# Performance work log

Hardware: AMD Instinct MI355X
Metric: run time of the kernel (lower is better)

The kernel has to match this reference:

```python
import jax, jax.numpy as jnp
import numpy as np

# Static multi-scale pyramid (H, W per level); Nv = sum(H*W) = 13294
SPATIAL = np.array([[100, 100], [50, 50], [25, 25], [13, 13]], dtype=np.int64)
B, C, NH, NL, NP = 2, 256, 8, 4, 4
D = C // NH
TOT = NH * NL * NP


def setup_inputs() -> dict:
    key = jax.random.key(0)
    ks = jax.random.split(key, 10)
    Nv = int((SPATIAL[:, 0] * SPATIAL[:, 1]).sum())
    Nq = Nv
    query = jax.random.normal(ks[0], (B, Nq, C), dtype=jnp.float32)
    value = jax.random.normal(ks[1], (B, Nv, C), dtype=jnp.float32)
    reference_points = jax.random.uniform(ks[2], (B, Nq, NL, 2), minval=0.05, maxval=0.95, dtype=jnp.float32)
    spatial_shapes = jnp.asarray(SPATIAL)
    level_start_index = jnp.asarray(np.concatenate([[0], np.cumsum(SPATIAL[:, 0] * SPATIAL[:, 1])[:-1]]))
    # sampling_offsets: small random weight + the rotated-grid bias from _reset_parameters
    W_off = 0.01 * jax.random.normal(ks[3], (C, TOT * 2), dtype=jnp.float32)
    thetas = np.arange(NH, dtype=np.float64) * (2.0 * np.pi / NH)
    grid = np.stack([np.cos(thetas), np.sin(thetas)], -1)
    grid = grid / np.abs(grid).max(-1, keepdims=True)
    grid = np.tile(grid[:, None, None, :], (1, NL, NP, 1)) * (np.arange(NP) + 1)[None, None, :, None]
    b_off = jnp.asarray(grid.reshape(-1), dtype=jnp.float32)
    W_attn = 0.01 * jax.random.normal(ks[4], (C, TOT), dtype=jnp.float32)
    b_attn = jnp.zeros((TOT,), jnp.float32)
    W_val = jax.random.normal(ks[5], (C, C), dtype=jnp.float32) / np.sqrt(C)
    b_val = jnp.zeros((C,), jnp.float32)
    W_out = jax.random.normal(ks[6], (C, C), dtype=jnp.float32) / np.sqrt(C)
    b_out = jnp.zeros((C,), jnp.float32)
    return {"query": query, "value": value, "reference_points": reference_points,
            "spatial_shapes": spatial_shapes, "level_start_index": level_start_index,
            "W_off": W_off, "b_off": b_off, "W_attn": W_attn, "b_attn": b_attn,
            "W_val": W_val, "b_val": b_val, "W_out": W_out, "b_out": b_out}


def _bilinear(vl, loc, H, W):
    # vl: [B, h, H*W, D]; loc: [B, Nq, h, P, 2] normalized (x, y) in [0,1]
    # Matches F.grid_sample(mode='bilinear', padding_mode='zeros', align_corners=False)
    Bb, h, _, Dd = vl.shape
    Nq, P = loc.shape[1], loc.shape[3]
    x = loc[..., 0] * W - 0.5
    y = loc[..., 1] * H - 0.5
    x0 = jnp.floor(x)
    y0 = jnp.floor(y)
    fx = x - x0
    fy = y - y0
    out = jnp.zeros((Bb, h, Nq * P, Dd), vl.dtype)
    corners = ((0, 0, (1 - fx) * (1 - fy)), (1, 0, fx * (1 - fy)),
               (0, 1, (1 - fx) * fy), (1, 1, fx * fy))
    for dx, dy, w in corners:
        xi = x0 + dx
        yi = y0 + dy
        valid = (xi >= 0) & (xi < W) & (yi >= 0) & (yi < H)
        idx = (jnp.clip(yi, 0, H - 1) * W + jnp.clip(xi, 0, W - 1)).astype(jnp.int32)
        idx = idx.transpose(0, 2, 1, 3).reshape(Bb, h, Nq * P)          # [B,h,Nq*P]
        wv = (w * valid).transpose(0, 2, 1, 3).reshape(Bb, h, Nq * P)   # [B,h,Nq*P]
        g = jnp.take_along_axis(vl, idx[..., None], axis=2)             # [B,h,Nq*P,D]
        out = out + g * wv[..., None]
    return out.reshape(Bb, h, Nq, P, Dd)


def reference(query, value, reference_points, spatial_shapes, level_start_index,
              W_off, b_off, W_attn, b_attn, W_val, b_val, W_out, b_out):
    Bb, Nq, Cc = query.shape
    v = (value @ W_val + b_val).reshape(Bb, -1, NH, D)                  # [B,Nv,h,D]
    off = (query @ W_off + b_off).reshape(Bb, Nq, NH, NL, NP, 2)
    attn = jax.nn.softmax((query @ W_attn + b_attn).reshape(Bb, Nq, NH, NL * NP), axis=-1)
    attn = attn.reshape(Bb, Nq, NH, NL, NP)
    # offset normalizer is (W, H) per level
    norm = jnp.asarray(SPATIAL[:, ::-1].copy(), dtype=query.dtype)      # [L,2]
    loc = reference_points[:, :, None, :, None, :] + off / norm[None, None, None, :, None, :]
    starts = np.concatenate([[0], np.cumsum(SPATIAL[:, 0] * SPATIAL[:, 1])])
    out_acc = jnp.zeros((Bb, NH, Nq, D), query.dtype)
    for l in range(NL):
        H, W = int(SPATIAL[l, 0]), int(SPATIAL[l, 1])
        vl = v[:, int(starts[l]):int(starts[l + 1])].transpose(0, 2, 1, 3)  # [B,h,HW,D]
        samp = _bilinear(vl, loc[:, :, :, l], H, W)                     # [B,h,Nq,P,D]
        w_l = attn[:, :, :, l].transpose(0, 2, 1, 3)                    # [B,h,Nq,P]
        out_acc = out_acc + jnp.einsum('bhqpd,bhqp->bhqd', samp, w_l)
    out = out_acc.transpose(0, 2, 1, 3).reshape(Bb, Nq, Cc)
    return out @ W_out + b_out
```

## Files before the change

kernel.cpp:

```cpp
#include <hip/hip_runtime.h>
#include <hip/hip_bf16.h>

#define NQ  13294
#define NV  13294
#define BQ  26588

typedef __attribute__((ext_vector_type(8))) short short8;
typedef __attribute__((ext_vector_type(4))) float f32x4;

static __device__ __forceinline__ ushort f2bf(float f) {
    unsigned int x = __float_as_uint(f);
    unsigned int r = (x + 0x7fffu + ((x >> 16) & 1u)) >> 16;
    return (ushort)r;
}
static __device__ __forceinline__ uint cvtpk_bf16(float a, float b) {
    uint r;
    asm("v_cvt_pk_bf16_f32 %0, %1, %2" : "=v"(r) : "v"(a), "v"(b));
    return r;
}
static __device__ __forceinline__ uint cvtpk_f16(float a, float b) {
    uint r;
    asm("v_cvt_pkrtz_f16_f32 %0, %1, %2" : "=v"(r) : "v"(a), "v"(b));
    return r;
}
static __device__ __forceinline__ float f16lo(uint u) {
    _Float16 h; ushort t = (ushort)(u & 0xffffu);
    __builtin_memcpy(&h, &t, 2); return (float)h;
}
static __device__ __forceinline__ float f16hi(uint u) {
    _Float16 h; ushort t = (ushort)(u >> 16);
    __builtin_memcpy(&h, &t, 2); return (float)h;
}
static __device__ __forceinline__ float fmamix_ll(float acc, uint g, uint w) {
    asm("v_fma_mix_f32 %0, %1, %2, %0 op_sel:[0,0,0] op_sel_hi:[1,1,0]" : "+v"(acc) : "v"(g), "v"(w));
    return acc;
}
static __device__ __forceinline__ float fmamix_hl(float acc, uint g, uint w) {
    asm("v_fma_mix_f32 %0, %1, %2, %0 op_sel:[1,0,0] op_sel_hi:[1,1,0]" : "+v"(acc) : "v"(g), "v"(w));
    return acc;
}
static __device__ __forceinline__ float fmamix_lh(float acc, uint g, uint w) {
    asm("v_fma_mix_f32 %0, %1, %2, %0 op_sel:[0,1,0] op_sel_hi:[1,1,0]" : "+v"(acc) : "v"(g), "v"(w));
    return acc;
}
static __device__ __forceinline__ float fmamix_hh(float acc, uint g, uint w) {
    asm("v_fma_mix_f32 %0, %1, %2, %0 op_sel:[1,1,0] op_sel_hi:[1,1,0]" : "+v"(acc) : "v"(g), "v"(w));
    return acc;
}
static __device__ __forceinline__ void gload_lds16(const void* g, void* l) {
    __builtin_amdgcn_global_load_lds(
        (const __attribute__((address_space(1))) uint*)g,
        (__attribute__((address_space(3))) uint*)l, 16, 0, 0);
}

__global__ __launch_bounds__(256) void prep_weights(
    const float* __restrict__ Wv, const float* __restrict__ Wo,
    const float* __restrict__ Wa, const float* __restrict__ Wu,
    const float* __restrict__ bo, const float* __restrict__ ba,
    ushort* __restrict__ tWv, ushort* __restrict__ tWoa,
    ushort* __restrict__ tWu, float* __restrict__ boa) {
    const int blk = blockIdx.x;
    const int tid = threadIdx.x;
    if (blk == 56) {
        if (tid < 256) boa[tid] = bo[tid];
        int j = tid + 256;
        if (j < 384) boa[j] = ba[j - 256];
        return;
    }
    __shared__ float t[64][65];
    const float* src; ushort* dst; int srcN, k0, n0, drow0;
    if (blk < 16)      { int u = blk;      src = Wv; srcN = 256; dst = tWv;  k0 = (u >> 2) * 64; n0 = (u & 3) * 64; drow0 = n0; }
    else if (blk < 32) { int u = blk - 16; src = Wo; srcN = 256; dst = tWoa; k0 = (u >> 2) * 64; n0 = (u & 3) * 64; drow0 = n0; }
    else if (blk < 40) { int u = blk - 32; src = Wa; srcN = 128; dst = tWoa; k0 = (u >> 1) * 64; n0 = (u & 1) * 64; drow0 = 256 + n0; }
    else               { int u = blk - 40; src = Wu; srcN = 256; dst = tWu;  k0 = (u >> 2) * 64; n0 = (u & 3) * 64; drow0 = n0; }
#pragma unroll
    for (int it = 0; it < 16; ++it) {
        int idx = tid + it * 256, r = idx >> 6, c = idx & 63;
        t[r][c] = src[(size_t)(k0 + r) * srcN + n0 + c];
    }
    __syncthreads();
#pragma unroll
    for (int it = 0; it < 16; ++it) {
        int idx = tid + it * 256, r = idx >> 6, c = idx & 63;
        dst[(size_t)(drow0 + r) * 256 + k0 + c] = f2bf(t[c][r]);
    }
}

#define ALDP 40
template<int AF32>
static __device__ __forceinline__ void gemm_core3(
    const void* __restrict__ Aptr, const ushort* __restrict__ Bt,
    const float* __restrict__ bias, void* __restrict__ Cout,
    int M, int N, int out_mode, int mblk, int nblk,
    ushort* sA, ushort* sB) {
    const int tid = threadIdx.x;
    const int wid = tid >> 6;
    const int lane = tid & 63;
    const int row0 = mblk * 128;
    const int col0 = nblk * 128;
    const int wr = (wid >> 1) * 64;
    const int wc = (wid & 1) * 64;

    f32x4 acc[4][4];
#pragma unroll
    for (int m = 0; m < 4; ++m)
#pragma unroll
        for (int n = 0; n < 4; ++n) acc[m][n] = (f32x4){0.f, 0.f, 0.f, 0.f};

    const int r0 = tid >> 2;
    const int seg = tid & 3;
    float4 rf[4];

    auto GLB = [&](int t) {
        int buf = t & 1;
#pragma unroll
        for (int i = 0; i < 2; ++i) {
            int rloc = 32 * wid + 16 * i;
            const char* gp = (const char*)Bt + ((size_t)(col0 + rloc + (lane >> 2))) * 512 + t * 64 + (lane & 3) * 16;
            gload_lds16(gp, (char*)sB + buf * 8192 + rloc * 64);
        }
    };
    auto GLA = [&](int t) {
        int buf = t & 1;
#pragma unroll
        for (int i = 0; i < 2; ++i) {
            int rloc = 32 * wid + 16 * i;
            const char* gp = (const char*)Aptr + ((size_t)(row0 + rloc + (lane >> 2))) * 512 + t * 64 + (lane & 3) * 16;
            gload_lds16(gp, (char*)sA + buf * 8192 + rloc * 64);
        }
    };
    auto REGLOAD = [&](int t) {
        int kk = t * 32;
#pragma unroll
        for (int it = 0; it < 2; ++it) {
            int gr = row0 + r0 + it * 64; gr = gr < M ? gr : M - 1;
            const float* Af = (const float*)Aptr + (size_t)gr * 256 + kk + seg * 8;
            rf[2 * it]     = *reinterpret_cast<const float4*>(Af);
            rf[2 * it + 1] = *reinterpret_cast<const float4*>(Af + 4);
        }
    };
    auto STOREA = [&](int t) {
        int buf = t & 1;
#pragma unroll
        for (int it = 0; it < 2; ++it) {
            int r = r0 + it * 64;
            uint4 wa;
            wa.x = cvtpk_bf16(rf[2 * it].x, rf[2 * it].y);
            wa.y = cvtpk_bf16(rf[2 * it].z, rf[2 * it].w);
            wa.z = cvtpk_bf16(rf[2 * it + 1].x, rf[2 * it + 1].y);
            wa.w = cvtpk_bf16(rf[2 * it + 1].z, rf[2 * it + 1].w);
            *reinterpret_cast<uint4*>(&sA[buf * (128 * ALDP) + r * ALDP + seg * 8]) = wa;
        }
    };
    auto COMPUTE = [&](int t) {
        int buf = t & 1;
        const int rbase = lane & 15;
        const int g8 = (lane >> 4) * 8;
        short8 a[4], b[4];
#pragma unroll
        for (int m = 0; m < 4; ++m) {
            int R = wr + m * 16 + rbase;
            a[m] = AF32
                ? *reinterpret_cast<const short8*>(&sA[buf * (128 * ALDP) + R * ALDP + g8])
                : *reinterpret_cast<const short8*>(&sA[buf * 4096 + R * 32 + g8]);
        }
#pragma unroll
        for (int n = 0; n < 4; ++n) {
            int R = wc + n * 16 + rbase;
            b[n] = *reinterpret_cast<const short8*>(&sB[buf * 4096 + R * 32 + g8]);
        }
#pragma unroll
        for (int m = 0; m < 4; ++m)
#pragma unroll
            for (int n = 0; n < 4; ++n)
                acc[m][n] = __builtin_amdgcn_mfma_f32_16x16x32_bf16(a[m], b[n], acc[m][n], 0, 0, 0);
    };

    if (AF32) { GLB(0); REGLOAD(0); STOREA(0); }
    else      { GLB(0); GLA(0); }
#pragma unroll
    for (int t = 0; t < 8; ++t) {
        __syncthreads();
        if (t < 7) {
            GLB(t + 1);
            if (AF32) REGLOAD(t + 1); else GLA(t + 1);
        }
        COMPUTE(t);
        if (AF32 && t < 7) STOREA(t + 1);
    }

    const int lr = (lane >> 4) * 4;
    const int lc = lane & 15;
#pragma unroll
    for (int m = 0; m < 4; ++m) {
#pragma unroll
        for (int n = 0; n < 4; ++n) {
            int gcol = col0 + wc + n * 16 + lc;
            float bv = bias[gcol];
#pragma unroll
            for (int j = 0; j < 4; ++j) {
                int grow = row0 + wr + m * 16 + lr + j;
                if (grow < M) {
                    float vv = acc[m][n][j] + bv;
                    if (out_mode == 0) {
                        ((float*)Cout)[(size_t)grow * N + gcol] = vv;
                    } else if (out_mode == 2) {
                        ((ushort*)Cout)[(size_t)grow * N + gcol] = (ushort)(cvtpk_f16(vv, vv) & 0xffffu);
                    } else {
                        int bb = grow >= NV;
                        int pix = grow - bb * NV;
                        int h = gcol >> 5, ch = gcol & 31;
                        ((ushort*)Cout)[(((size_t)(bb * 8 + h)) * NV + pix) * 32 + ch] =
                            (ushort)(cvtpk_f16(vv, vv) & 0xffffu);
                    }
                }
            }
        }
    }
}

__global__ __launch_bounds__(256, 3) void gemm_fused(
    const float* __restrict__ value, const float* __restrict__ query,
    const ushort* __restrict__ tWv, const ushort* __restrict__ tWoa,
    const float* __restrict__ bval, const float* __restrict__ boa,
    ushort* __restrict__ vproj_t, ushort* __restrict__ offattn) {
    __shared__ ushort sA[2 * 128 * ALDP];
    __shared__ ushort sB[2 * 4096];
    const bool g1 = blockIdx.y < 2;
    gemm_core3<1>(g1 ? (const void*)value : (const void*)query,
                  g1 ? tWv : tWoa, g1 ? bval : boa,
                  g1 ? (void*)vproj_t : (void*)offattn,
                  BQ, g1 ? 256 : 384, g1 ? 3 : 2,
                  blockIdx.x, g1 ? blockIdx.y : blockIdx.y - 2, sA, sB);
}

__global__ __launch_bounds__(256, 4) void gemm_out(
    const ushort* __restrict__ outacc, const ushort* __restrict__ tWu,
    const float* __restrict__ bout, float* __restrict__ dout) {
    __shared__ ushort sA[2 * 4096];
    __shared__ ushort sB[2 * 4096];
    gemm_core3<0>(outacc, tWu, bout, dout, BQ, 256, 0, blockIdx.x, blockIdx.y, sA, sB);
}

__global__ __launch_bounds__(256, 4) void msda_sample(
    const ushort* __restrict__ offattn,
    const float* __restrict__ refp,
    const ushort* __restrict__ vt,
    ushort* __restrict__ out_acc) {
    __shared__ int2 s_ad[4][256];
    __shared__ uint s_w[4][256];

    const int tid = threadIdx.x;
    const int qi = tid >> 6;
    const int lane = tid & 63;
    const int bq = blockIdx.x * 4 + qi;
    const int b = bq / NQ;
    const int q = bq - b * NQ;
    const int h = lane >> 3;

    const ushort* oa = offattn + (size_t)bq * 384;
    const int t0 = lane * 2;
    uint lgu = *reinterpret_cast<const uint*>(oa + 256 + t0);
    float lg0 = f16lo(lgu), lg1 = f16hi(lgu);
    float m = fmaxf(lg0, lg1);
    m = fmaxf(m, __shfl_xor(m, 1));
    m = fmaxf(m, __shfl_xor(m, 2));
    m = fmaxf(m, __shfl_xor(m, 4));
    float e0 = __expf(lg0 - m), e1 = __expf(lg1 - m);
    float ssum = e0 + e1;
    ssum += __shfl_xor(ssum, 1);
    ssum += __shfl_xor(ssum, 2);
    ssum += __shfl_xor(ssum, 4);
    float inv = 1.f / ssum;

    uint2 offu = *reinterpret_cast<const uint2*>(oa + 2 * t0);
    const int l = (t0 >> 2) & 3;
    const int   Wi = (l == 0) ? 100 : (l == 1) ? 50 : (l == 2) ? 25 : 13;
    const int   st = (l == 0) ? 0 : (l == 1) ? 10000 : (l == 2) ? 12500 : 13125;
    const float Wf = (float)Wi;
    float rx = refp[(((size_t)b * NQ + q) * 4 + l) * 2 + 0];
    float ry = refp[(((size_t)b * NQ + q) * 4 + l) * 2 + 1];
    const int vbase = (b * 8 + h) * NV * 64;

#pragma unroll
    for (int j = 0; j < 2; ++j) {
        float e = (j ? e1 : e0) * inv;
        float ox = j ? f16lo(offu.y) : f16lo(offu.x);
        float oy = j ? f16hi(offu.y) : f16hi(offu.x);
        float x = fmaf(rx, Wf, ox) - 0.5f;
        float y = fmaf(ry, Wf, oy) - 0.5f;
        float x0f = floorf(x), y0f = floorf(y);
        float fx = x - x0f, fy = y - y0f;
        int x0 = (int)x0f, y0 = (int)y0f;
        float wx0 = (x0 >= 0 && x0 < Wi)         ? e * (1.f - fx) : 0.f;
        float wx1 = (x0 + 1 >= 0 && x0 + 1 < Wi) ? e * fx         : 0.f;
        float wy0 = (y0 >= 0 && y0 < Wi)         ? (1.f - fy) : 0.f;
        float wy1 = (y0 + 1 >= 0 && y0 + 1 < Wi) ? fy         : 0.f;
        int px0 = min(max(x0, 0), Wi - 1) * 64;
        int px1 = min(max(x0 + 1, 0), Wi - 1) * 64;
        int a0 = vbase + (st + min(max(y0, 0), Wi - 1) * Wi) * 64;
        int a1 = vbase + (st + min(max(y0 + 1, 0), Wi - 1) * Wi) * 64;
        int s = 2 * (lane & 7) + j;
        int u = ((s ^ h) << 4) + (h << 1);
        s_ad[qi][u]     = make_int2(a0 + px0, a1 + px0);
        s_ad[qi][u + 1] = make_int2(a0 + px1, a1 + px1);
        s_w[qi][u]      = cvtpk_f16(wx0 * wy0, wx0 * wy1);
        s_w[qi][u + 1]  = cvtpk_f16(wx1 * wy0, wx1 * wy1);
    }
    __syncthreads();

    const int xbit = (lane >> 2) & 1;
    const int cg16 = (lane & 3) * 16;
    const char* vtc = (const char*)vt;

    int2 A[16]; uint Wp[16];
#pragma unroll
    for (int ss = 0; ss < 16; ++ss) {
        int u = ((ss ^ h) << 4) + (h << 1) + xbit;
        int2 a = s_ad[qi][u];
        A[ss] = make_int2(a.x + cg16, a.y + cg16);
        Wp[ss] = s_w[qi][u];
    }

    float acc[8] = {0.f, 0.f, 0.f, 0.f, 0.f, 0.f, 0.f, 0.f};
#pragma unroll
    for (int ss = 0; ss < 16; ++ss) {
        uint4 g0 = *reinterpret_cast<const uint4*>(vtc + (uint)A[ss].x);
        uint4 g1 = *reinterpret_cast<const uint4*>(vtc + (uint)A[ss].y);
        uint w = Wp[ss];
        acc[0] = fmamix_ll(acc[0], g0.x, w); acc[1] = fmamix_hl(acc[1], g0.x, w);
        acc[2] = fmamix_ll(acc[2], g0.y, w); acc[3] = fmamix_hl(acc[3], g0.y, w);
        acc[4] = fmamix_ll(acc[4], g0.z, w); acc[5] = fmamix_hl(acc[5], g0.z, w);
        acc[6] = fmamix_ll(acc[6], g0.w, w); acc[7] = fmamix_hl(acc[7], g0.w, w);
        acc[0] = fmamix_lh(acc[0], g1.x, w); acc[1] = fmamix_hh(acc[1], g1.x, w);
        acc[2] = fmamix_lh(acc[2], g1.y, w); acc[3] = fmamix_hh(acc[3], g1.y, w);
        acc[4] = fmamix_lh(acc[4], g1.z, w); acc[5] = fmamix_hh(acc[5], g1.z, w);
        acc[6] = fmamix_lh(acc[6], g1.w, w); acc[7] = fmamix_hh(acc[7], g1.w, w);
    }

#pragma unroll
    for (int i = 0; i < 8; ++i) acc[i] += __shfl_xor(acc[i], 4);
    if (xbit == 0) {
        uint4 o;
        o.x = cvtpk_bf16(acc[0], acc[1]);
        o.y = cvtpk_bf16(acc[2], acc[3]);
        o.z = cvtpk_bf16(acc[4], acc[5]);
        o.w = cvtpk_bf16(acc[6], acc[7]);
        *reinterpret_cast<uint4*>(out_acc + (size_t)bq * 256 + h * 32 + (lane & 3) * 8) = o;
    }
}

extern "C" void kernel_launch(void* const* d_in, const int* in_sizes, int n_in,
                              void* d_out, int out_size, void* d_ws, size_t ws_size,
                              hipStream_t stream) {
    const float* query  = (const float*)d_in[0];
    const float* value  = (const float*)d_in[1];
    const float* refp   = (const float*)d_in[2];
    const float* W_off  = (const float*)d_in[5];
    const float* b_off  = (const float*)d_in[6];
    const float* W_attn = (const float*)d_in[7];
    const float* b_attn = (const float*)d_in[8];
    const float* W_val  = (const float*)d_in[9];
    const float* b_val  = (const float*)d_in[10];
    const float* W_out  = (const float*)d_in[11];
    const float* b_out  = (const float*)d_in[12];

    const size_t ROWB = (size_t)BQ * 256 * 2;
    char* ws = (char*)d_ws;
    ushort* vproj_t = (ushort*)(ws);
    ushort* outacc  = (ushort*)(ws + ROWB);
    ushort* offattn = (ushort*)(ws + 2 * ROWB);
    char*   wbase   = ws + 2 * ROWB + (size_t)BQ * 384 * 2;
    ushort* tWv  = (ushort*)(wbase);
    ushort* tWoa = tWv + 65536;
    ushort* tWu  = tWoa + 98304;
    float*  boa  = (float*)(tWu + 65536);

    prep_weights<<<57, 256, 0, stream>>>(
        W_val, W_off, W_attn, W_out, b_off, b_attn, tWv, tWoa, tWu, boa);

    gemm_fused<<<dim3(208, 5), 256, 0, stream>>>(
        value, query, tWv, tWoa, b_val, boa, vproj_t, offattn);

    msda_sample<<<BQ / 4, 256, 0, stream>>>(offattn, refp, vproj_t, outacc);

    gemm_out<<<dim3(208, 2), 256, 0, stream>>>(outacc, tWu, b_out, (float*)d_out);
}
```

Baseline: 108.6 us.

## Pre-convert value/query to bf16 and use swizzled direct-to-LDS GEMM loads

The fp32 value and query tensors are converted to bf16 in extra blocks of the weight-prep kernel. The fused projection GEMM can then stream its A operand with global_load_lds instead of register loads plus in-kernel conversion, and its occupancy target rises to 4. Both A and B LDS tiles use an XOR-style rotation swizzle to cut bank conflicts, and rows are clamped at M. The cost is an extra pass that writes and re-reads about 27 MB of bf16 through the workspace, while the GEMM fetches half as many A bytes as before.

```diff
diff --git a/kernel.cpp b/kernel.cpp
--- a/kernel.cpp
+++ b/kernel.cpp
@@ -4,6 +4,7 @@
 #define NQ  13294
 #define NV  13294
 #define BQ  26588
+#define NEL 6806528
 
 typedef __attribute__((ext_vector_type(8))) short short8;
 typedef __attribute__((ext_vector_type(4))) float f32x4;
@@ -53,14 +54,31 @@
         (__attribute__((address_space(3))) uint*)l, 16, 0, 0);
 }
 
-__global__ __launch_bounds__(256) void prep_weights(
+__global__ __launch_bounds__(256) void prep_all(
     const float* __restrict__ Wv, const float* __restrict__ Wo,
     const float* __restrict__ Wa, const float* __restrict__ Wu,
     const float* __restrict__ bo, const float* __restrict__ ba,
+    const float* __restrict__ value, const float* __restrict__ query,
     ushort* __restrict__ tWv, ushort* __restrict__ tWoa,
-    ushort* __restrict__ tWu, float* __restrict__ boa) {
+    ushort* __restrict__ tWu, float* __restrict__ boa,
+    ushort* __restrict__ v_bf, ushort* __restrict__ q_bf) {
     const int blk = blockIdx.x;
     const int tid = threadIdx.x;
+    if (blk >= 57) {
+        int i8 = (blk - 57) * 2048 + tid * 8;
+        const float* src; ushort* dst; int off;
+        if (i8 < NEL) { src = value; dst = v_bf; off = i8; }
+        else          { src = query; dst = q_bf; off = i8 - NEL; }
+        float4 f0 = *reinterpret_cast<const float4*>(src + off);
+        float4 f1 = *reinterpret_cast<const float4*>(src + off + 4);
+        uint4 o;
+        o.x = cvtpk_bf16(f0.x, f0.y);
+        o.y = cvtpk_bf16(f0.z, f0.w);
+        o.z = cvtpk_bf16(f1.x, f1.y);
+        o.w = cvtpk_bf16(f1.z, f1.w);
+        *reinterpret_cast<uint4*>(dst + off) = o;
+        return;
+    }
     if (blk == 56) {
         if (tid < 256) boa[tid] = bo[tid];
         int j = tid + 256;
@@ -86,10 +104,8 @@
     }
 }
 
-#define ALDP 40
-template<int AF32>
-static __device__ __forceinline__ void gemm_core3(
-    const void* __restrict__ Aptr, const ushort* __restrict__ Bt,
+static __device__ __forceinline__ void gemm_core4(
+    const ushort* __restrict__ Ab, const ushort* __restrict__ Bt,
     const float* __restrict__ bias, void* __restrict__ Cout,
     int M, int N, int out_mode, int mblk, int nblk,
     ushort* sA, ushort* sB) {
@@ -107,67 +123,38 @@
 #pragma unroll
         for (int n = 0; n < 4; ++n) acc[m][n] = (f32x4){0.f, 0.f, 0.f, 0.f};
 
-    const int r0 = tid >> 2;
-    const int seg = tid & 3;
-    float4 rf[4];
-
-    auto GLB = [&](int t) {
+    auto GL = [&](int t) {
         int buf = t & 1;
 #pragma unroll
         for (int i = 0; i < 2; ++i) {
-            int rloc = 32 * wid + 16 * i;
-            const char* gp = (const char*)Bt + ((size_t)(col0 + rloc + (lane >> 2))) * 512 + t * 64 + (lane & 3) * 16;
-            gload_lds16(gp, (char*)sB + buf * 8192 + rloc * 64);
-        }
-    };
-    auto GLA = [&](int t) {
-        int buf = t & 1;
-#pragma unroll
-        for (int i = 0; i < 2; ++i) {
-            int rloc = 32 * wid + 16 * i;
-            const char* gp = (const char*)Aptr + ((size_t)(row0 + rloc + (lane >> 2))) * 512 + t * 64 + (lane & 3) * 16;
-            gload_lds16(gp, (char*)sA + buf * 8192 + rloc * 64);
-        }
-    };
-    auto REGLOAD = [&](int t) {
-        int kk = t * 32;
-#pragma unroll
-        for (int it = 0; it < 2; ++it) {
-            int gr = row0 + r0 + it * 64; gr = gr < M ? gr : M - 1;
-            const float* Af = (const float*)Aptr + (size_t)gr * 256 + kk + seg * 8;
-            rf[2 * it]     = *reinterpret_cast<const float4*>(Af);
-            rf[2 * it + 1] = *reinterpret_cast<const float4*>(Af + 4);
-        }
-    };
-    auto STOREA = [&](int t) {
-        int buf = t & 1;
-#pragma unroll
-        for (int it = 0; it < 2; ++it) {
-            int r = r0 + it * 64;
-            uint4 wa;
-            wa.x = cvtpk_bf16(rf[2 * it].x, rf[2 * it].y);
-            wa.y = cvtpk_bf16(rf[2 * it].z, rf[2 * it].w);
-            wa.z = cvtpk_bf16(rf[2 * it + 1].x, rf[2 * it + 1].y);
-            wa.w = cvtpk_bf16(rf[2 * it + 1].z, rf[2 * it + 1].w);
-            *reinterpret_cast<uint4*>(&sA[buf * (128 * ALDP) + r * ALDP + seg * 8]) = wa;
+            int rbase16 = 32 * wid + 16 * i;
+            int rloc = rbase16 + (lane >> 2);
+            int csrc = ((lane & 3) - (rloc >> 1)) & 3;
+            size_t koff = (size_t)t * 64 + csrc * 16;
+            int gr = row0 + rloc; gr = gr < M ? gr : M - 1;
+            gload_lds16((const char*)Ab + (size_t)gr * 512 + koff,
+                        (char*)sA + buf * 8192 + rbase16 * 64);
+            int gc = col0 + rloc;
+            gload_lds16((const char*)Bt + (size_t)gc * 512 + koff,
+                        (char*)sB + buf * 8192 + rbase16 * 64);
         }
     };
     auto COMPUTE = [&](int t) {
         int buf = t & 1;
         const int rbase = lane & 15;
-        const int g8 = (lane >> 4) * 8;
+        const int g = lane >> 4;
         short8 a[4], b[4];
 #pragma unroll
         for (int m = 0; m < 4; ++m) {
             int R = wr + m * 16 + rbase;
-            a[m] = AF32
-                ? *reinterpret_cast<const short8*>(&sA[buf * (128 * ALDP) + R * ALDP + g8])
-                : *reinterpret_cast<const short8*>(&sA[buf * 4096 + R * 32 + g8]);
+            a[m] = *reinterpret_cast<const short8*>(
+                (char*)sA + buf * 8192 + R * 64 + (((g + (R >> 1)) & 3) << 4));
         }
 #pragma unroll
         for (int n = 0; n < 4; ++n) {
             int R = wc + n * 16 + rbase;
-            b[n] = *reinterpret_cast<const short8*>(&sB[buf * 4096 + R * 32 + g8]);
+            b[n] = *reinterpret_cast<const short8*>(
+                (char*)sB + buf * 8192 + R * 64 + (((g + (R >> 1)) & 3) << 4));
         }
 #pragma unroll
         for (int m = 0; m < 4; ++m)
@@ -176,17 +163,12 @@
                 acc[m][n] = __builtin_amdgcn_mfma_f32_16x16x32_bf16(a[m], b[n], acc[m][n], 0, 0, 0);
     };
 
-    if (AF32) { GLB(0); REGLOAD(0); STOREA(0); }
-    else      { GLB(0); GLA(0); }
+    GL(0);
 #pragma unroll
     for (int t = 0; t < 8; ++t) {
         __syncthreads();
-        if (t < 7) {
-            GLB(t + 1);
-            if (AF32) REGLOAD(t + 1); else GLA(t + 1);
-        }
+        if (t < 7) GL(t + 1);
         COMPUTE(t);
-        if (AF32 && t < 7) STOREA(t + 1);
     }
 
     const int lr = (lane >> 4) * 4;
@@ -219,19 +201,18 @@
     }
 }
 
-__global__ __launch_bounds__(256, 3) void gemm_fused(
-    const float* __restrict__ value, const float* __restrict__ query,
+__global__ __launch_bounds__(256, 4) void gemm_fused(
+    const ushort* __restrict__ v_bf, const ushort* __restrict__ q_bf,
     const ushort* __restrict__ tWv, const ushort* __restrict__ tWoa,
     const float* __restrict__ bval, const float* __restrict__ boa,
     ushort* __restrict__ vproj_t, ushort* __restrict__ offattn) {
-    __shared__ ushort sA[2 * 128 * ALDP];
+    __shared__ ushort sA[2 * 4096];
     __shared__ ushort sB[2 * 4096];
     const bool g1 = blockIdx.y < 2;
-    gemm_core3<1>(g1 ? (const void*)value : (const void*)query,
-                  g1 ? tWv : tWoa, g1 ? bval : boa,
-                  g1 ? (void*)vproj_t : (void*)offattn,
-                  BQ, g1 ? 256 : 384, g1 ? 3 : 2,
-                  blockIdx.x, g1 ? blockIdx.y : blockIdx.y - 2, sA, sB);
+    gemm_core4(g1 ? v_bf : q_bf, g1 ? tWv : tWoa, g1 ? bval : boa,
+               g1 ? (void*)vproj_t : (void*)offattn,
+               BQ, g1 ? 256 : 384, g1 ? 3 : 2,
+               blockIdx.x, g1 ? blockIdx.y : blockIdx.y - 2, sA, sB);
 }
 
 __global__ __launch_bounds__(256, 4) void gemm_out(
@@ -239,7 +220,7 @@
     const float* __restrict__ bout, float* __restrict__ dout) {
     __shared__ ushort sA[2 * 4096];
     __shared__ ushort sB[2 * 4096];
-    gemm_core3<0>(outacc, tWu, bout, dout, BQ, 256, 0, blockIdx.x, blockIdx.y, sA, sB);
+    gemm_core4(outacc, tWu, bout, dout, BQ, 256, 0, blockIdx.x, blockIdx.y, sA, sB);
 }
 
 __global__ __launch_bounds__(256, 4) void msda_sample(
@@ -369,18 +350,21 @@
     char* ws = (char*)d_ws;
     ushort* vproj_t = (ushort*)(ws);
     ushort* outacc  = (ushort*)(ws + ROWB);
-    ushort* offattn = (ushort*)(ws + 2 * ROWB);
-    char*   wbase   = ws + 2 * ROWB + (size_t)BQ * 384 * 2;
+    ushort* v_bf    = (ushort*)(ws + 2 * ROWB);
+    ushort* q_bf    = (ushort*)(ws + 3 * ROWB);
+    ushort* offattn = (ushort*)(ws + 4 * ROWB);
+    char*   wbase   = ws + 4 * ROWB + (size_t)BQ * 384 * 2;
     ushort* tWv  = (ushort*)(wbase);
     ushort* tWoa = tWv + 65536;
     ushort* tWu  = tWoa + 98304;
     float*  boa  = (float*)(tWu + 65536);
 
-    prep_weights<<<57, 256, 0, stream>>>(
-        W_val, W_off, W_attn, W_out, b_off, b_attn, tWv, tWoa, tWu, boa);
+    prep_all<<<57 + 6647, 256, 0, stream>>>(
+        W_val, W_off, W_attn, W_out, b_off, b_attn, value, query,
+        tWv, tWoa, tWu, boa, v_bf, q_bf);
 
     gemm_fused<<<dim3(208, 5), 256, 0, stream>>>(
-        value, query, tWv, tWoa, b_val, boa, vproj_t, offattn);
+        v_bf, q_bf, tWv, tWoa, b_val, boa, vproj_t, offattn);
 
     msda_sample<<<BQ / 4, 256, 0, stream>>>(offattn, refp, vproj_t, outacc);
 
```

Measured after the change: 111.2 us. 2.4% more time.
